# Performance work log

Measured on AMD Instinct MI355X. Metric: run time of the kernel, lower is better.

## Reference

```python
import jax, jax.numpy as jnp
import numpy as np

BATCH, DIM, REPS = 4096, 2048, 8


def setup_inputs() -> dict:
    key = jax.random.key(0)
    ks = jax.random.split(key, 6)
    x = jax.random.normal(ks[0], (BATCH, DIM), jnp.float32)
    theta = 0.5 * jax.random.normal(ks[1], (DIM, REPS + 1, 2), jnp.float32)
    preacts_weight = 1.0 + 0.1 * jax.random.normal(ks[2], (DIM, REPS), jnp.float32)
    preacts_bias = 0.1 * jax.random.normal(ks[3], (DIM, REPS), jnp.float32)
    postact_weights = 1.0 + 0.1 * jax.random.normal(ks[4], (DIM,), jnp.float32)
    postact_bias = 0.1 * jax.random.normal(ks[5], (DIM,), jnp.float32)
    return dict(x=x, theta=theta, preacts_weight=preacts_weight,
                preacts_bias=preacts_bias, postact_weights=postact_weights,
                postact_bias=postact_bias)


def _rz(psi, ang):
    # RZ = diag(exp(-i*ang/2), exp(+i*ang/2)); ang broadcasts over (b, dim)
    ph = jnp.exp(ang * (-0.5j))  # complex64
    return jnp.stack([psi[..., 0] * ph, psi[..., 1] * jnp.conj(ph)], axis=-1)


def _ry(psi, ang):
    # RY = [[cos, -sin], [sin, cos]] with half-angle
    c = jnp.cos(0.5 * ang)
    s = jnp.sin(0.5 * ang)
    a, b = psi[..., 0], psi[..., 1]
    return jnp.stack([c * a - s * b, s * a + c * b], axis=-1)


def reference(x, theta, preacts_weight, preacts_bias, postact_weights, postact_bias):
    reps = theta.shape[1] - 1
    batch, dim = x.shape
    # encoded angles per rep: (reps, b, dim)
    enc = preacts_weight.T[:, None, :] * x[None] + preacts_bias.T[:, None, :]
    # |0> then Hadamard -> (1/sqrt2)(|0> + |1>) per (batch, dim) qubit
    inv_sqrt2 = jnp.asarray(1.0 / np.sqrt(2.0), jnp.complex64)
    psi0 = jnp.full((batch, dim, 2), inv_sqrt2, jnp.complex64)
    th0 = theta[:, :reps, 0].T  # (reps, dim)
    th1 = theta[:, :reps, 1].T  # (reps, dim)

    def step(psi, xs):
        t0, t1, e = xs
        psi = _rz(psi, t0)   # trainable RZ, (dim,) broadcast over batch
        psi = _ry(psi, t1)   # trainable RY
        psi = _rz(psi, e)    # data re-uploading RZ, (b, dim)
        return psi, None

    psi, _ = jax.lax.scan(step, psi0, (th0, th1, enc))
    psi = _rz(psi, theta[:, reps, 0])
    psi = _ry(psi, theta[:, reps, 1])
    # <Z> = |psi_0|^2 - |psi_1|^2, real float32
    z = (psi[..., 0].real ** 2 + psi[..., 0].imag ** 2) - \
        (psi[..., 1].real ** 2 + psi[..., 1].imag ** 2)
    return z * postact_weights + postact_bias
```

## Files before the change

kernel.cpp:

```cpp
#include <hip/hip_runtime.h>
#include <math.h>

constexpr int BATCH = 4096;
constexpr int DIM   = 2048;
constexpr int REPS  = 8;
constexpr float INV2PI = 0.15915494309189535f;

constexpr int TPB   = 256;
constexpr int GRIDX = DIM / TPB;
constexpr int GRIDY = 128;
constexpr int BPB   = BATCH / GRIDY;

__device__ __forceinline__ void poly_sincos(float f, float& s, float& c) {
    const float m = __builtin_rintf(f);
    const float r = f - m;
    const float u = r * r;
    float p = fmaf(32.7680000f, u, -74.4701952f);
    p = fmaf(p, u, 81.3660160f);
    p = fmaf(p, u, -41.3311104f);
    p = fmaf(p, u, 6.2830536f);
    s = p * r;
    float q = fmaf(45.6130560f, u, -82.3881728f);
    q = fmaf(q, u, 64.6713088f);
    q = fmaf(q, u, -19.7309120f);
    c = fmaf(q, u, 0.9999527f);
}

__global__ __launch_bounds__(TPB, 4)
void daruan_kernel(const float* __restrict__ x,
                   const float* __restrict__ theta,
                   const float* __restrict__ paw,
                   const float* __restrict__ pab,
                   const float* __restrict__ postw,
                   const float* __restrict__ postb,
                   float* __restrict__ out)
{
    const int d = blockIdx.x * TPB + threadIdx.x;

    const float* th = theta + (size_t)d * 18;
    const float t00 = th[0] * INV2PI;
    const float X0  = __builtin_amdgcn_cosf(t00);
    const float Y0  = __builtin_amdgcn_sinf(t00);
    const float t10 = th[1] * INV2PI;
    const float Xi  = X0 * __builtin_amdgcn_cosf(t10);
    const float Yi  = Y0;
    const float Zi  = -X0 * __builtin_amdgcn_sinf(t10);

    float cy[REPS], sy[REPS], wr[REPS], br[REPS];
#pragma unroll
    for (int k = 0; k < REPS; ++k) {
        const float t1 = th[2 * k + 3] * INV2PI;
        cy[k] = __builtin_amdgcn_cosf(t1);
        sy[k] = __builtin_amdgcn_sinf(t1);
        wr[k] = paw[(size_t)d * REPS + k] * INV2PI;
        br[k] = (pab[(size_t)d * REPS + k] + th[2 * (k + 1)]) * INV2PI;
    }
    const float pw = postw[d];
    const float pb = postb[d];

    const int bbase = blockIdx.y * BPB;
    const float* xp = x + (size_t)bbase * DIM + d;
    float* op = out + (size_t)bbase * DIM + d;

    auto fill = [&](float xv, float (&seh)[4], float (&ceh)[4]) {
#pragma unroll
        for (int j = 0; j < 4; ++j) {
            const float e = fmaf(wr[2 * j], xv, br[2 * j]);
            seh[j] = __builtin_amdgcn_sinf(e);
            ceh[j] = __builtin_amdgcn_cosf(e);
        }
    };
    auto consume = [&](float xv, const float (&seh)[4], const float (&ceh)[4]) -> float {
        float sep[4], cep[4];
#pragma unroll
        for (int j = 0; j < 4; ++j)
            poly_sincos(fmaf(wr[2 * j + 1], xv, br[2 * j + 1]), sep[j], cep[j]);

        float X = fmaf(Xi, ceh[0], -Yi * seh[0]);
        float Y = fmaf(Xi, seh[0],  Yi * ceh[0]);
        float Z = Zi;
#pragma unroll
        for (int r = 1; r < REPS; ++r) {
            const float se = (r & 1) ? sep[r >> 1] : seh[r >> 1];
            const float ce = (r & 1) ? cep[r >> 1] : ceh[r >> 1];
            const float Xb = fmaf(X, cy[r - 1],  Z * sy[r - 1]);
            const float Zb = fmaf(Z, cy[r - 1], -X * sy[r - 1]);
            X = fmaf(Xb, ce, -Y * se);
            if (r < REPS - 1)
                Y = fmaf(Xb, se, Y * ce);
            Z = Zb;
        }
        return fmaf(Z, cy[REPS - 1], -X * sy[REPS - 1]);
    };

    float seA[4], ceA[4], seB[4], ceB[4];
    float xA = xp[0];
    fill(xA, seA, ceA);
    float xB = xp[DIM];

#pragma unroll 1
    for (int c = 0; c < BPB; c += 2) {
        fill(xB, seB, ceB);
        const float z0 = consume(xA, seA, ceA);
        op[(size_t)c * DIM] = fmaf(z0, pw, pb);
        const float xn = xp[(size_t)((c + 2) & (BPB - 1)) * DIM];
        fill(xn, seA, ceA);
        const float z1 = consume(xB, seB, ceB);
        op[(size_t)(c + 1) * DIM] = fmaf(z1, pw, pb);
        xA = xn;
        xB = xp[(size_t)((c + 3) & (BPB - 1)) * DIM];
    }
}

extern "C" void kernel_launch(void* const* d_in, const int* in_sizes, int n_in,
                              void* d_out, int out_size, void* d_ws, size_t ws_size,
                              hipStream_t stream) {
    const float* x     = (const float*)d_in[0];
    const float* theta = (const float*)d_in[1];
    const float* paw   = (const float*)d_in[2];
    const float* pab   = (const float*)d_in[3];
    const float* postw = (const float*)d_in[4];
    const float* postb = (const float*)d_in[5];
    float* out = (float*)d_out;

    daruan_kernel<<<dim3(GRIDX, GRIDY), dim3(TPB), 0, stream>>>(
        x, theta, paw, pab, postw, postb, out);
}
```

Before: 34.46 us.

## Replace software-pipelined fill/consume loop with ILP-2 chunks and double grid rows

The explicit software pipeline, which computed the hardware sin/cos of the next element while the current one was consumed, is replaced by a simpler loop. Each iteration prefetches the next two x values and then evaluates two independent elements, leaving interleaving to the compiler. GRIDY doubles to 256, halving the batch rows per block and doubling block count for better latency hiding and load balance. The cost is losing the hand-arranged overlap of transcendental and polynomial work, plus more redundant per-block setup of the theta-derived constants.

```diff
diff --git a/kernel.cpp b/kernel.cpp
--- a/kernel.cpp
+++ b/kernel.cpp
@@ -8,8 +8,10 @@
 
 constexpr int TPB   = 256;
 constexpr int GRIDX = DIM / TPB;
-constexpr int GRIDY = 128;
+constexpr int GRIDY = 256;
 constexpr int BPB   = BATCH / GRIDY;
+constexpr int ILP   = 2;
+constexpr int NCH   = BPB / ILP;
 
 __device__ __forceinline__ void poly_sincos(float f, float& s, float& c) {
     const float m = __builtin_rintf(f);
@@ -62,20 +64,18 @@
     const float* xp = x + (size_t)bbase * DIM + d;
     float* op = out + (size_t)bbase * DIM + d;
 
-    auto fill = [&](float xv, float (&seh)[4], float (&ceh)[4]) {
+    auto do_elem = [&](float xv) -> float {
+        float seh[4], ceh[4];
 #pragma unroll
         for (int j = 0; j < 4; ++j) {
             const float e = fmaf(wr[2 * j], xv, br[2 * j]);
             seh[j] = __builtin_amdgcn_sinf(e);
             ceh[j] = __builtin_amdgcn_cosf(e);
         }
-    };
-    auto consume = [&](float xv, const float (&seh)[4], const float (&ceh)[4]) -> float {
         float sep[4], cep[4];
 #pragma unroll
         for (int j = 0; j < 4; ++j)
             poly_sincos(fmaf(wr[2 * j + 1], xv, br[2 * j + 1]), sep[j], cep[j]);
-
         float X = fmaf(Xi, ceh[0], -Yi * seh[0]);
         float Y = fmaf(Xi, seh[0],  Yi * ceh[0]);
         float Z = Zi;
@@ -93,23 +93,25 @@
         return fmaf(Z, cy[REPS - 1], -X * sy[REPS - 1]);
     };
 
-    float seA[4], ceA[4], seB[4], ceB[4];
-    float xA = xp[0];
-    fill(xA, seA, ceA);
-    float xB = xp[DIM];
+    float xv[ILP];
+#pragma unroll
+    for (int i = 0; i < ILP; ++i) xv[i] = xp[(size_t)i * DIM];
 
 #pragma unroll 1
-    for (int c = 0; c < BPB; c += 2) {
-        fill(xB, seB, ceB);
-        const float z0 = consume(xA, seA, ceA);
-        op[(size_t)c * DIM] = fmaf(z0, pw, pb);
-        const float xn = xp[(size_t)((c + 2) & (BPB - 1)) * DIM];
-        fill(xn, seA, ceA);
-        const float z1 = consume(xB, seB, ceB);
-        op[(size_t)(c + 1) * DIM] = fmaf(z1, pw, pb);
-        xA = xn;
-        xB = xp[(size_t)((c + 3) & (BPB - 1)) * DIM];
+    for (int cc = 0; cc < NCH - 1; ++cc) {
+        float xn[ILP];
+#pragma unroll
+        for (int i = 0; i < ILP; ++i)
+            xn[i] = xp[(size_t)((cc + 1) * ILP + i) * DIM];
+#pragma unroll
+        for (int i = 0; i < ILP; ++i)
+            op[(size_t)(cc * ILP + i) * DIM] = fmaf(do_elem(xv[i]), pw, pb);
+#pragma unroll
+        for (int i = 0; i < ILP; ++i) xv[i] = xn[i];
     }
+#pragma unroll
+    for (int i = 0; i < ILP; ++i)
+        op[(size_t)((NCH - 1) * ILP + i) * DIM] = fmaf(do_elem(xv[i]), pw, pb);
 }
 
 extern "C" void kernel_launch(void* const* d_in, const int* in_sizes, int n_in,
```

Measured after the change: 35.50 us. 3.0% more time.
